# Optimization experiments

Hardware: AMD Instinct MI355X
Metric: run time of the kernel (lower is better)

## Reference

```python
import jax, jax.numpy as jnp
import numpy as np

N, E = 100000, 1600000
IN_DIM, HID, NCLS = 64, 128, 18
BATCH, K = 8, 5000


def setup_inputs() -> dict:
    key = jax.random.key(0)
    ks = jax.random.split(key, 9)
    features = jax.random.normal(ks[0], (N, IN_DIM), dtype=jnp.float32)
    src = jax.random.randint(ks[1], (E,), 0, N, dtype=jnp.int32)
    dst = jax.random.randint(ks[2], (E,), 0, N, dtype=jnp.int32)
    def glorot(k, shape):
        lim = float(np.sqrt(6.0 / (shape[0] + shape[1])))
        return jax.random.uniform(k, shape, jnp.float32, -lim, lim)
    W1 = glorot(ks[3], (IN_DIM, HID)); b1 = jnp.zeros((HID,), jnp.float32)
    W2 = glorot(ks[4], (HID, HID));    b2 = jnp.zeros((HID,), jnp.float32)
    W3 = glorot(ks[5], (K * HID, NCLS)); b3 = jnp.zeros((NCLS,), jnp.float32)
    return {"features": features, "src": src, "dst": dst,
            "W1": W1, "b1": b1, "W2": W2, "b2": b2, "W3": W3, "b3": b3}


def reference(features, src, dst, W1, b1, W2, b2, W3, b3):
    n = features.shape[0]
    ones = jnp.ones(src.shape[0], features.dtype)
    out_deg = jax.ops.segment_sum(ones, src, num_segments=n)
    in_deg = jax.ops.segment_sum(ones, dst, num_segments=n)
    norm_src = jnp.clip(out_deg, 1.0) ** -0.5  # DGL norm='both'
    norm_dst = jnp.clip(in_deg, 1.0) ** -0.5

    def gconv(x, W, b, act):
        h = (x @ W) * norm_src[:, None]          # transform then normalize src
        agg = jax.ops.segment_sum(h[src], dst, num_segments=n)  # gather+scatter-add
        agg = agg * norm_dst[:, None] + b
        return jax.nn.relu(agg) if act else agg

    h = gconv(features, W1, b1, True)   # [N, HID]
    h = gconv(h, W2, b2, True)          # [N, HID]

    # global_sort_pool: equal-sized graphs of N//BATCH nodes, top-K by last channel
    n_per = n // BATCH
    hb = h.reshape(BATCH, n_per, HID)
    _, idx = jax.lax.top_k(hb[..., -1], K)                  # [B, K] descending
    topk = jnp.take_along_axis(hb, idx[..., None], axis=1)  # [B, K, HID]
    pooled = topk.reshape(BATCH, K * HID)

    return pooled @ W3 + b3  # [B, NCLS]
```

## Files before the change

### kernel.cpp

```cpp
#include <hip/hip_runtime.h>
#include <cstdint>
#include <cstddef>

#define N_NODES 100000
#define N_EDGES 1600000
#define IN_DIM  64
#define HID     128
#define NCLS    18
#define BATCH   8
#define TOPK    5000
#define NPER    12500
#define SORTN   16384
#define SORTC   2048

#define BSHIFT  9
#define BNODES  (1 << BSHIFT)
#define NBUCK   ((N_NODES + BNODES - 1) / BNODES)
#define CHUNK   8192


__global__ __launch_bounds__(256) void k_bcount(const int* __restrict__ src,
                                                const int* __restrict__ dst,
                                                int* __restrict__ bcntS,
                                                int* __restrict__ bcntD) {
    __shared__ int cs[NBUCK], cd[NBUCK];
    for (int b = threadIdx.x; b < NBUCK; b += 256) { cs[b] = 0; cd[b] = 0; }
    __syncthreads();
    const int base = blockIdx.x * CHUNK;
    const int end  = min(base + CHUNK, N_EDGES);
    for (int e = base + threadIdx.x; e < end; e += 256) {
        atomicAdd(&cs[src[e] >> BSHIFT], 1);
        atomicAdd(&cd[dst[e] >> BSHIFT], 1);
    }
    __syncthreads();
    for (int b = threadIdx.x; b < NBUCK; b += 256) {
        if (cs[b]) atomicAdd(&bcntS[b], cs[b]);
        if (cd[b]) atomicAdd(&bcntD[b], cd[b]);
    }
}

__global__ void k_bscan(const int* __restrict__ bcntS, const int* __restrict__ bcntD,
                        int* __restrict__ baseS, int* __restrict__ baseD,
                        int* __restrict__ curS, int* __restrict__ curD) {
    if (threadIdx.x == 0 && blockIdx.x == 0) {
        int rs = 0, rd = 0;
        for (int b = 0; b < NBUCK; ++b) {
            baseS[b] = rs; curS[b] = rs; rs += bcntS[b];
            baseD[b] = rd; curD[b] = rd; rd += bcntD[b];
        }
        baseS[NBUCK] = rs; baseD[NBUCK] = rd;
    }
}


__global__ __launch_bounds__(256) void k_bin2(const int* __restrict__ src,
                                              const int* __restrict__ dst,
                                              int* __restrict__ cursorD,
                                              int* __restrict__ cursorS,
                                              unsigned* __restrict__ binbuf,
                                              unsigned* __restrict__ sbin) {
    __shared__ int cD[NBUCK], gD[NBUCK], aD[NBUCK];
    __shared__ int cS[NBUCK], gS[NBUCK], aS[NBUCK];
    const int base = blockIdx.x * CHUNK;
    const int end  = min(base + CHUNK, N_EDGES);
    for (int b = threadIdx.x; b < NBUCK; b += 256) {
        cD[b] = 0; aD[b] = 0; cS[b] = 0; aS[b] = 0;
    }
    __syncthreads();
    for (int e = base + threadIdx.x; e < end; e += 256) {
        atomicAdd(&cD[dst[e] >> BSHIFT], 1);
        atomicAdd(&cS[src[e] >> BSHIFT], 1);
    }
    __syncthreads();
    for (int b = threadIdx.x; b < NBUCK; b += 256) {
        if (cD[b] > 0) gD[b] = atomicAdd(&cursorD[b], cD[b]);
        if (cS[b] > 0) gS[b] = atomicAdd(&cursorS[b], cS[b]);
    }
    __syncthreads();
    for (int e = base + threadIdx.x; e < end; e += 256) {
        int d = dst[e], s = src[e];
        int bd = d >> BSHIFT;
        int od = atomicAdd(&aD[bd], 1);
        binbuf[gD[bd] + od] = ((unsigned)(d & (BNODES - 1)) << 17) | (unsigned)s;
        int bs = s >> BSHIFT;
        int os = atomicAdd(&aS[bs], 1);
        sbin[gS[bs] + os] = (unsigned)(s & (BNODES - 1));
    }
}


__global__ __launch_bounds__(256) void k_hist_all(const unsigned* __restrict__ sbin,
                                                  const int* __restrict__ baseS,
                                                  const unsigned* __restrict__ binbuf,
                                                  const int* __restrict__ baseD,
                                                  float* __restrict__ normS,
                                                  float* __restrict__ normD,
                                                  int* __restrict__ row_ptr,
                                                  int* __restrict__ ssrc) {
    __shared__ int cnt[BNODES];
    __shared__ int tmp[BNODES];
    const int nodeBase = blockIdx.x << BSHIFT;
    for (int t = threadIdx.x; t < BNODES; t += 256) cnt[t] = 0;
    __syncthreads();
    {
        const int beg = baseS[blockIdx.x], end = baseS[blockIdx.x + 1];
        for (int e = beg + threadIdx.x; e < end; e += 256)
            atomicAdd(&cnt[sbin[e]], 1);
    }
    __syncthreads();
    for (int t = threadIdx.x; t < BNODES; t += 256) {
        int node = nodeBase + t;
        if (node < N_NODES)
            normS[node] = 1.0f / sqrtf((float)max(cnt[t], 1));
        cnt[t] = 0;
    }
    __syncthreads();
    const int beg = baseD[blockIdx.x], end = baseD[blockIdx.x + 1];
    for (int e = beg + threadIdx.x; e < end; e += 256)
        atomicAdd(&cnt[binbuf[e] >> 17], 1);
    __syncthreads();
    for (int t = threadIdx.x; t < BNODES; t += 256) {
        int node = nodeBase + t;
        if (node < N_NODES)
            normD[node] = 1.0f / sqrtf((float)max(cnt[t], 1));
    }
    for (int s = 1; s < BNODES; s <<= 1) {
        for (int t = threadIdx.x; t < BNODES; t += 256)
            tmp[t] = (t >= s) ? cnt[t - s] + cnt[t] : cnt[t];
        __syncthreads();
        for (int t = threadIdx.x; t < BNODES; t += 256) cnt[t] = tmp[t];
        __syncthreads();
    }
    for (int t = threadIdx.x; t < BNODES; t += 256) {
        int b = beg + ((t == 0) ? 0 : cnt[t - 1]);
        tmp[t] = b;
        int node = nodeBase + t;
        if (node < N_NODES) row_ptr[node] = b;
    }
    if (blockIdx.x == 0 && threadIdx.x == 0) row_ptr[N_NODES] = N_EDGES;
    __syncthreads();
    for (int e = beg + threadIdx.x; e < end; e += 256) {
        unsigned v = binbuf[e];
        int pos = atomicAdd(&tmp[v >> 17], 1);
        ssrc[pos] = (int)(v & 0x1FFFFu);
    }
}


#define BMT 64
#define BKT 32

template<int KDIM, bool SCALE, bool POST, bool KEYS>
__global__ __launch_bounds__(256) void k_fused(const float* __restrict__ X,
                                               const int* __restrict__ row_ptr,
                                               const int* __restrict__ ssrc,
                                               const float* __restrict__ normSrc,
                                               const float* __restrict__ W,
                                               const float* __restrict__ normD,
                                               const float* __restrict__ bias,
                                               const float* __restrict__ normS_post,
                                               float* __restrict__ keys,
                                               float* __restrict__ out) {
    __shared__ float xs[BMT][KDIM + 4];
    __shared__ float ws[BKT * HID];

    const int tid = threadIdx.x;
    const int rt = blockIdx.x * BMT;

    {
        constexpr int LPN = KDIM / 4;
        constexpr int NCH = 256 / LPN;
        const int w = tid / LPN;
        const int lane = tid % LPN;
        const float4* __restrict__ hv = (const float4*)X;
        #pragma unroll
        for (int c = 0; c < BMT / NCH; ++c) {
            const int row = c * NCH + w;
            const int node = rt + row;
            float4 a4 = make_float4(0.f, 0.f, 0.f, 0.f);
            if (node < N_NODES) {
                const int beg = row_ptr[node], end = row_ptr[node + 1];
                int e = beg;
                for (; e + 4 <= end; e += 4) {
                    int s0 = ssrc[e + 0], s1 = ssrc[e + 1], s2 = ssrc[e + 2], s3 = ssrc[e + 3];
                    float4 v0 = hv[(size_t)s0 * LPN + lane];
                    float4 v1 = hv[(size_t)s1 * LPN + lane];
                    float4 v2 = hv[(size_t)s2 * LPN + lane];
                    float4 v3 = hv[(size_t)s3 * LPN + lane];
                    if constexpr (SCALE) {
                        float n0 = normSrc[s0], n1 = normSrc[s1], n2 = normSrc[s2], n3 = normSrc[s3];
                        a4.x += v0.x * n0; a4.y += v0.y * n0; a4.z += v0.z * n0; a4.w += v0.w * n0;
                        a4.x += v1.x * n1; a4.y += v1.y * n1; a4.z += v1.z * n1; a4.w += v1.w * n1;
                        a4.x += v2.x * n2; a4.y += v2.y * n2; a4.z += v2.z * n2; a4.w += v2.w * n2;
                        a4.x += v3.x * n3; a4.y += v3.y * n3; a4.z += v3.z * n3; a4.w += v3.w * n3;
                    } else {
                        a4.x += v0.x; a4.y += v0.y; a4.z += v0.z; a4.w += v0.w;
                        a4.x += v1.x; a4.y += v1.y; a4.z += v1.z; a4.w += v1.w;
                        a4.x += v2.x; a4.y += v2.y; a4.z += v2.z; a4.w += v2.w;
                        a4.x += v3.x; a4.y += v3.y; a4.z += v3.z; a4.w += v3.w;
                    }
                }
                for (; e < end; ++e) {
                    int s0 = ssrc[e];
                    float4 v0 = hv[(size_t)s0 * LPN + lane];
                    if constexpr (SCALE) {
                        float n0 = normSrc[s0];
                        a4.x += v0.x * n0; a4.y += v0.y * n0; a4.z += v0.z * n0; a4.w += v0.w * n0;
                    } else {
                        a4.x += v0.x; a4.y += v0.y; a4.z += v0.z; a4.w += v0.w;
                    }
                }
            }
            *(float4*)&xs[row][lane * 4] = a4;
        }
    }

    const int tx = tid & 31;
    const int ty = tid >> 5;
    const int col0 = tx * 4;
    const int row0 = ty * 8;

    float acc[8][4];
    #pragma unroll
    for (int r = 0; r < 8; ++r)
        #pragma unroll
        for (int c = 0; c < 4; ++c) acc[r][c] = 0.f;

    for (int k0 = 0; k0 < KDIM; k0 += BKT) {
        __syncthreads();
        {
            const float4* wsrc = (const float4*)(W + (size_t)k0 * HID);
            #pragma unroll
            for (int i = tid; i < BKT * HID / 4; i += 256)
                ((float4*)ws)[i] = wsrc[i];
        }
        __syncthreads();
        #pragma unroll 4
        for (int k = 0; k < BKT; ++k) {
            float4 b = *(const float4*)&ws[k * HID + col0];
            float a[8];
            #pragma unroll
            for (int r = 0; r < 8; ++r) a[r] = xs[row0 + r][k0 + k];
            #pragma unroll
            for (int r = 0; r < 8; ++r) {
                acc[r][0] += a[r] * b.x;
                acc[r][1] += a[r] * b.y;
                acc[r][2] += a[r] * b.z;
                acc[r][3] += a[r] * b.w;
            }
        }
    }

    const float4 bb = *(const float4*)(bias + col0);
    #pragma unroll
    for (int r = 0; r < 8; ++r) {
        int gr = rt + row0 + r;
        if (gr < N_NODES) {
            float nd = normD[gr];
            float4 o;
            o.x = fmaxf(acc[r][0] * nd + bb.x, 0.f);
            o.y = fmaxf(acc[r][1] * nd + bb.y, 0.f);
            o.z = fmaxf(acc[r][2] * nd + bb.z, 0.f);
            o.w = fmaxf(acc[r][3] * nd + bb.w, 0.f);
            if (KEYS && col0 == 124) keys[gr] = o.w;
            if (POST) {
                float ns = normS_post[gr];
                o.x *= ns; o.y *= ns; o.z *= ns; o.w *= ns;
            }
            *(float4*)(out + (size_t)gr * HID + col0) = o;
        }
    }
}


__global__ __launch_bounds__(256) void k_sort_init(const float* __restrict__ keys,
                                                   unsigned long long* __restrict__ arr) {
    int i = blockIdx.x * 256 + threadIdx.x;
    if (i >= BATCH * SORTN) return;
    int g = i >> 14;
    int l = i & (SORTN - 1);
    unsigned long long c;
    if (l < NPER) {
        unsigned u = __float_as_uint(keys[g * NPER + l]);
        unsigned s = (u & 0x80000000u) ? ~u : (u | 0x80000000u);
        unsigned d = ~s;
        c = ((unsigned long long)d << 32) | (unsigned)l;
    } else {
        c = 0xFFFFFFFFFFFFFFFFull;
    }
    arr[i] = c;
}

__global__ __launch_bounds__(1024) void k_sort_local_full(unsigned long long* __restrict__ arr) {
    __shared__ unsigned long long lds[SORTC];
    const int base  = blockIdx.x * SORTC;
    const int gbase = base & (SORTN - 1);
    lds[threadIdx.x]        = arr[base + threadIdx.x];
    lds[threadIdx.x + 1024] = arr[base + threadIdx.x + 1024];
    __syncthreads();
    for (int k = 2; k <= SORTC; k <<= 1) {
        for (int j = k >> 1; j > 0; j >>= 1) {
            int t = threadIdx.x;
            int i = ((t & ~(j - 1)) << 1) | (t & (j - 1));
            bool up = (((gbase + i) & k) == 0);
            unsigned long long a = lds[i], b = lds[i + j];
            if ((a > b) == up) { lds[i] = b; lds[i + j] = a; }
            __syncthreads();
        }
    }
    arr[base + threadIdx.x]        = lds[threadIdx.x];
    arr[base + threadIdx.x + 1024] = lds[threadIdx.x + 1024];
}

__global__ __launch_bounds__(256) void k_sort_global(unsigned long long* __restrict__ arr,
                                                     int k, int j) {
    int tg = blockIdx.x * 256 + threadIdx.x;
    if (tg >= BATCH * (SORTN / 2)) return;
    int g = tg >> 13;
    int t = tg & (SORTN / 2 - 1);
    int i = ((t & ~(j - 1)) << 1) | (t & (j - 1));
    bool up = ((i & k) == 0);
    unsigned long long* p = arr + (size_t)g * SORTN;
    unsigned long long a = p[i], b = p[i + j];
    if ((a > b) == up) { p[i] = b; p[i + j] = a; }
}

__global__ __launch_bounds__(1024) void k_sort_local_tail(unsigned long long* __restrict__ arr,
                                                          int k) {
    __shared__ unsigned long long lds[SORTC];
    const int base  = blockIdx.x * SORTC;
    const int gbase = base & (SORTN - 1);
    lds[threadIdx.x]        = arr[base + threadIdx.x];
    lds[threadIdx.x + 1024] = arr[base + threadIdx.x + 1024];
    __syncthreads();
    for (int j = SORTC >> 1; j > 0; j >>= 1) {
        int t = threadIdx.x;
        int i = ((t & ~(j - 1)) << 1) | (t & (j - 1));
        bool up = (((gbase + i) & k) == 0);
        unsigned long long a = lds[i], b = lds[i + j];
        if ((a > b) == up) { lds[i] = b; lds[i + j] = a; }
        __syncthreads();
    }
    arr[base + threadIdx.x]        = lds[threadIdx.x];
    arr[base + threadIdx.x + 1024] = lds[threadIdx.x + 1024];
}

__global__ __launch_bounds__(256) void k_sort_emit(const unsigned long long* __restrict__ arr,
                                                   int* __restrict__ topk_idx,
                                                   const float* __restrict__ b3,
                                                   float* __restrict__ out) {
    int i = blockIdx.x * 256 + threadIdx.x;
    if (i < BATCH * NCLS) out[i] = b3[i % NCLS];
    if (i >= BATCH * TOPK) return;
    int b = i / TOPK;
    int k = i - b * TOPK;
    topk_idx[i] = (int)(arr[(size_t)b * SORTN + k] & 0xFFFFFFFFull);
}


#define KPB 100

__global__ __launch_bounds__(128) void k_final(const float* __restrict__ h2,
                                               const int* __restrict__ topk_idx,
                                               const float* __restrict__ W3,
                                               float* __restrict__ out) {
    __shared__ float red[128 * NCLS];
    const int b = blockIdx.x / (TOPK / KPB);
    const int chunk = blockIdx.x % (TOPK / KPB);
    const int j = threadIdx.x;
    float acc[NCLS];
    #pragma unroll
    for (int c = 0; c < NCLS; ++c) acc[c] = 0.f;
    const int k0 = chunk * KPB;
    for (int k = k0; k < k0 + KPB; ++k) {
        int node = b * NPER + topk_idx[b * TOPK + k];
        float h = h2[(size_t)node * HID + j];
        const float* wrow = W3 + (size_t)(k * HID + j) * NCLS;
        #pragma unroll
        for (int c = 0; c < NCLS; ++c) acc[c] += h * wrow[c];
    }
    #pragma unroll
    for (int c = 0; c < NCLS; ++c) red[j * NCLS + c] = acc[c];
    __syncthreads();
    for (int s = 64; s > 0; s >>= 1) {
        if (j < s) {
            #pragma unroll
            for (int c = 0; c < NCLS; ++c) red[j * NCLS + c] += red[(j + s) * NCLS + c];
        }
        __syncthreads();
    }
    if (j < NCLS) atomicAdd(&out[b * NCLS + j], red[j]);
}


extern "C" void kernel_launch(void* const* d_in, const int* in_sizes, int n_in,
                              void* d_out, int out_size, void* d_ws, size_t ws_size,
                              hipStream_t stream) {
    const float* features = (const float*)d_in[0];
    const int*   src      = (const int*)d_in[1];
    const int*   dst      = (const int*)d_in[2];
    const float* W1       = (const float*)d_in[3];
    const float* b1       = (const float*)d_in[4];
    const float* W2       = (const float*)d_in[5];
    const float* b2       = (const float*)d_in[6];
    const float* W3       = (const float*)d_in[7];
    const float* b3       = (const float*)d_in[8];
    float* out = (float*)d_out;

    char* p = (char*)d_ws;
    auto carve = [&](size_t bytes) -> void* {
        void* r = (void*)p;
        p += (bytes + 511) & ~(size_t)511;
        return r;
    };
    float* normS     = (float*)carve((size_t)N_NODES * 4);
    float* normD     = (float*)carve((size_t)N_NODES * 4);
    int*   row_ptr   = (int*)carve((size_t)(N_NODES + 1) * 4);
    int*   bcntS     = (int*)carve((size_t)NBUCK * 4);
    int*   bcntD     = (int*)carve((size_t)NBUCK * 4);
    int*   baseS     = (int*)carve((size_t)(NBUCK + 1) * 4);
    int*   baseD     = (int*)carve((size_t)(NBUCK + 1) * 4);
    int*   curS      = (int*)carve((size_t)NBUCK * 4);
    int*   curD      = (int*)carve((size_t)NBUCK * 4);
    int*   ssrc      = (int*)carve((size_t)N_EDGES * 4);
    unsigned* binbuf = (unsigned*)carve((size_t)N_EDGES * 4);
    unsigned* sbin   = (unsigned*)carve((size_t)N_EDGES * 4);
    float* keys      = (float*)carve((size_t)N_NODES * 4);
    int*   topk_idx  = (int*)carve((size_t)BATCH * TOPK * 4);
    unsigned long long* sortbuf = (unsigned long long*)carve((size_t)BATCH * SORTN * 8);
    float* bufA      = (float*)carve((size_t)N_NODES * HID * 4);
    float* bufB      = (float*)carve((size_t)N_NODES * HID * 4);

    const int GB = (N_NODES + BMT - 1) / BMT;
    const int BB = (N_EDGES + CHUNK - 1) / CHUNK;

    hipMemsetAsync(bcntS, 0, (size_t)NBUCK * 4, stream);
    hipMemsetAsync(bcntD, 0, (size_t)NBUCK * 4, stream);

    k_bcount<<<BB, 256, 0, stream>>>(src, dst, bcntS, bcntD);
    k_bscan<<<1, 64, 0, stream>>>(bcntS, bcntD, baseS, baseD, curS, curD);
    k_bin2<<<BB, 256, 0, stream>>>(src, dst, curD, curS, binbuf, sbin);
    k_hist_all<<<NBUCK, 256, 0, stream>>>(sbin, baseS, binbuf, baseD,
                                          normS, normD, row_ptr, ssrc);

    k_fused<IN_DIM, true, true, false><<<GB, 256, 0, stream>>>(
        features, row_ptr, ssrc, normS, W1, normD, b1, normS, nullptr, bufA);
    k_fused<HID, false, false, true><<<GB, 256, 0, stream>>>(
        bufA, row_ptr, ssrc, nullptr, W2, normD, b2, nullptr, keys, bufB);

    const int NCHUNK = BATCH * SORTN / SORTC;
    const int GCE    = (BATCH * (SORTN / 2) + 255) / 256;
    k_sort_init<<<(BATCH * SORTN + 255) / 256, 256, 0, stream>>>(keys, sortbuf);
    k_sort_local_full<<<NCHUNK, 1024, 0, stream>>>(sortbuf);
    k_sort_global<<<GCE, 256, 0, stream>>>(sortbuf, 4096, 2048);
    k_sort_local_tail<<<NCHUNK, 1024, 0, stream>>>(sortbuf, 4096);
    k_sort_global<<<GCE, 256, 0, stream>>>(sortbuf, 8192, 4096);
    k_sort_global<<<GCE, 256, 0, stream>>>(sortbuf, 8192, 2048);
    k_sort_local_tail<<<NCHUNK, 1024, 0, stream>>>(sortbuf, 8192);
    k_sort_global<<<GCE, 256, 0, stream>>>(sortbuf, 16384, 8192);
    k_sort_global<<<GCE, 256, 0, stream>>>(sortbuf, 16384, 4096);
    k_sort_global<<<GCE, 256, 0, stream>>>(sortbuf, 16384, 2048);
    k_sort_local_tail<<<NCHUNK, 1024, 0, stream>>>(sortbuf, 16384);
    k_sort_emit<<<(BATCH * TOPK + 255) / 256, 256, 0, stream>>>(sortbuf, topk_idx, b3, out);

    k_final<<<BATCH * (TOPK / KPB), 128, 0, stream>>>(bufB, topk_idx, W3, out);
}
```

Before: 583.6 us.

## Split layer-2 fused aggregate+GEMM into separate gather kernel and tiled GEMM

The second graph conv layer previously ran as one fused kernel in which each 64-node block gathered neighbor rows into shared memory and then multiplied by W2. It is now split into a warp-per-node aggregation kernel writing to a global buffer, followed by a standalone tiled GEMM that applies the norm, bias and ReLU and extracts the sort keys. This gives the irregular gather its own launch shape, with small blocks and more parallelism, and avoids the large shared-memory tile that limited occupancy in the fused version. The cost is an extra round trip of the 100000x128 aggregated tensor through global memory, plus one more launch.

Measured after the change: 578.4 us. About the same (-0.9%).

```diff
diff --git a/kernel.cpp b/kernel.cpp
--- a/kernel.cpp
+++ b/kernel.cpp
@@ -150,25 +150,22 @@
 #define BMT 64
 #define BKT 32
 
-template<int KDIM, bool SCALE, bool POST, bool KEYS>
-__global__ __launch_bounds__(256) void k_fused(const float* __restrict__ X,
-                                               const int* __restrict__ row_ptr,
-                                               const int* __restrict__ ssrc,
-                                               const float* __restrict__ normSrc,
-                                               const float* __restrict__ W,
-                                               const float* __restrict__ normD,
-                                               const float* __restrict__ bias,
-                                               const float* __restrict__ normS_post,
-                                               float* __restrict__ keys,
-                                               float* __restrict__ out) {
-    __shared__ float xs[BMT][KDIM + 4];
+__global__ __launch_bounds__(256) void k_fused1(const float* __restrict__ X,
+                                                const int* __restrict__ row_ptr,
+                                                const int* __restrict__ ssrc,
+                                                const float* __restrict__ normS,
+                                                const float* __restrict__ W,
+                                                const float* __restrict__ normD,
+                                                const float* __restrict__ bias,
+                                                float* __restrict__ out) {
+    __shared__ float xs[BMT][IN_DIM + 4];
     __shared__ float ws[BKT * HID];
 
     const int tid = threadIdx.x;
     const int rt = blockIdx.x * BMT;
 
     {
-        constexpr int LPN = KDIM / 4;
+        constexpr int LPN = IN_DIM / 4;
         constexpr int NCH = 256 / LPN;
         const int w = tid / LPN;
         const int lane = tid % LPN;
@@ -183,32 +180,21 @@
                 int e = beg;
                 for (; e + 4 <= end; e += 4) {
                     int s0 = ssrc[e + 0], s1 = ssrc[e + 1], s2 = ssrc[e + 2], s3 = ssrc[e + 3];
+                    float n0 = normS[s0], n1 = normS[s1], n2 = normS[s2], n3 = normS[s3];
                     float4 v0 = hv[(size_t)s0 * LPN + lane];
                     float4 v1 = hv[(size_t)s1 * LPN + lane];
                     float4 v2 = hv[(size_t)s2 * LPN + lane];
                     float4 v3 = hv[(size_t)s3 * LPN + lane];
-                    if constexpr (SCALE) {
-                        float n0 = normSrc[s0], n1 = normSrc[s1], n2 = normSrc[s2], n3 = normSrc[s3];
-                        a4.x += v0.x * n0; a4.y += v0.y * n0; a4.z += v0.z * n0; a4.w += v0.w * n0;
-                        a4.x += v1.x * n1; a4.y += v1.y * n1; a4.z += v1.z * n1; a4.w += v1.w * n1;
-                        a4.x += v2.x * n2; a4.y += v2.y * n2; a4.z += v2.z * n2; a4.w += v2.w * n2;
-                        a4.x += v3.x * n3; a4.y += v3.y * n3; a4.z += v3.z * n3; a4.w += v3.w * n3;
-                    } else {
-                        a4.x += v0.x; a4.y += v0.y; a4.z += v0.z; a4.w += v0.w;
-                        a4.x += v1.x; a4.y += v1.y; a4.z += v1.z; a4.w += v1.w;
-                        a4.x += v2.x; a4.y += v2.y; a4.z += v2.z; a4.w += v2.w;
-                        a4.x += v3.x; a4.y += v3.y; a4.z += v3.z; a4.w += v3.w;
-                    }
+                    a4.x += v0.x * n0; a4.y += v0.y * n0; a4.z += v0.z * n0; a4.w += v0.w * n0;
+                    a4.x += v1.x * n1; a4.y += v1.y * n1; a4.z += v1.z * n1; a4.w += v1.w * n1;
+                    a4.x += v2.x * n2; a4.y += v2.y * n2; a4.z += v2.z * n2; a4.w += v2.w * n2;
+                    a4.x += v3.x * n3; a4.y += v3.y * n3; a4.z += v3.z * n3; a4.w += v3.w * n3;
                 }
                 for (; e < end; ++e) {
                     int s0 = ssrc[e];
+                    float n0 = normS[s0];
                     float4 v0 = hv[(size_t)s0 * LPN + lane];
-                    if constexpr (SCALE) {
-                        float n0 = normSrc[s0];
-                        a4.x += v0.x * n0; a4.y += v0.y * n0; a4.z += v0.z * n0; a4.w += v0.w * n0;
-                    } else {
-                        a4.x += v0.x; a4.y += v0.y; a4.z += v0.z; a4.w += v0.w;
-                    }
+                    a4.x += v0.x * n0; a4.y += v0.y * n0; a4.z += v0.z * n0; a4.w += v0.w * n0;
                 }
             }
             *(float4*)&xs[row][lane * 4] = a4;
@@ -226,7 +212,7 @@
         #pragma unroll
         for (int c = 0; c < 4; ++c) acc[r][c] = 0.f;
 
-    for (int k0 = 0; k0 < KDIM; k0 += BKT) {
+    for (int k0 = 0; k0 < IN_DIM; k0 += BKT) {
         __syncthreads();
         {
             const float4* wsrc = (const float4*)(W + (size_t)k0 * HID);
@@ -262,11 +248,115 @@
             o.y = fmaxf(acc[r][1] * nd + bb.y, 0.f);
             o.z = fmaxf(acc[r][2] * nd + bb.z, 0.f);
             o.w = fmaxf(acc[r][3] * nd + bb.w, 0.f);
-            if (KEYS && col0 == 124) keys[gr] = o.w;
-            if (POST) {
-                float ns = normS_post[gr];
-                o.x *= ns; o.y *= ns; o.z *= ns; o.w *= ns;
+            float ns = normS[gr];
+            o.x *= ns; o.y *= ns; o.z *= ns; o.w *= ns;
+            *(float4*)(out + (size_t)gr * HID + col0) = o;
+        }
+    }
+}
+
+
+#define ACC4(A, V) { A.x += V.x; A.y += V.y; A.z += V.z; A.w += V.w; }
+
+__global__ __launch_bounds__(256) void k_agg128(const float* __restrict__ hs,
+                                                const int* __restrict__ row_ptr,
+                                                const int* __restrict__ ssrc,
+                                                float* __restrict__ out) {
+    const int node = blockIdx.x * 8 + (threadIdx.x >> 5);
+    const int lane = threadIdx.x & 31;
+    if (node >= N_NODES) return;
+    const int beg = row_ptr[node], end = row_ptr[node + 1];
+    const float4* __restrict__ hv = (const float4*)hs;
+    float4 acc = make_float4(0.f, 0.f, 0.f, 0.f);
+    int e = beg;
+    for (; e + 4 <= end; e += 4) {
+        int s0 = ssrc[e + 0], s1 = ssrc[e + 1], s2 = ssrc[e + 2], s3 = ssrc[e + 3];
+        float4 v0 = hv[(size_t)s0 * 32 + lane];
+        float4 v1 = hv[(size_t)s1 * 32 + lane];
+        float4 v2 = hv[(size_t)s2 * 32 + lane];
+        float4 v3 = hv[(size_t)s3 * 32 + lane];
+        ACC4(acc, v0); ACC4(acc, v1); ACC4(acc, v2); ACC4(acc, v3);
+    }
+    for (; e < end; ++e) {
+        float4 v0 = hv[(size_t)ssrc[e] * 32 + lane];
+        ACC4(acc, v0);
+    }
+    *(float4*)(out + (size_t)node * HID + lane * 4) = acc;
+}
+
+
+__global__ __launch_bounds__(256) void k_gemm2(const float* __restrict__ X,
+                                               const float* __restrict__ W,
+                                               const float* __restrict__ normD,
+                                               const float* __restrict__ bias,
+                                               float* __restrict__ keys,
+                                               float* __restrict__ out) {
+    __shared__ float xs[BMT][BKT + 4];
+    __shared__ float ws[BKT * HID];
+
+    const int tid = threadIdx.x;
+    const int tx = tid & 31;
+    const int ty = tid >> 5;
+    const int col0 = tx * 4;
+    const int row0 = ty * 8;
+    const int rt = blockIdx.x * BMT;
+
+    float acc[8][4];
+    #pragma unroll
+    for (int r = 0; r < 8; ++r)
+        #pragma unroll
+        for (int c = 0; c < 4; ++c) acc[r][c] = 0.f;
+
+    for (int k0 = 0; k0 < HID; k0 += BKT) {
+        __syncthreads();
+        {
+            const float4* wsrc = (const float4*)(W + (size_t)k0 * HID);
+            #pragma unroll
+            for (int i = tid; i < BKT * HID / 4; i += 256)
+                ((float4*)ws)[i] = wsrc[i];
+        }
+        {
+            #pragma unroll
+            for (int i = tid; i < BMT * BKT / 4; i += 256) {
+                int row = i >> 3;
+                int kq  = i & 7;
+                int gr  = rt + row;
+                float4 v = make_float4(0.f, 0.f, 0.f, 0.f);
+                if (gr < N_NODES)
+                    v = *(const float4*)(X + (size_t)gr * HID + k0 + kq * 4);
+                *(float4*)&xs[row][kq * 4] = v;
             }
+        }
+        __syncthreads();
+
+        #pragma unroll 4
+        for (int k = 0; k < BKT; ++k) {
+            float4 b = *(const float4*)&ws[k * HID + col0];
+            float a[8];
+            #pragma unroll
+            for (int r = 0; r < 8; ++r) a[r] = xs[row0 + r][k];
+            #pragma unroll
+            for (int r = 0; r < 8; ++r) {
+                acc[r][0] += a[r] * b.x;
+                acc[r][1] += a[r] * b.y;
+                acc[r][2] += a[r] * b.z;
+                acc[r][3] += a[r] * b.w;
+            }
+        }
+    }
+
+    const float4 bb = *(const float4*)(bias + col0);
+    #pragma unroll
+    for (int r = 0; r < 8; ++r) {
+        int gr = rt + row0 + r;
+        if (gr < N_NODES) {
+            float nd = normD[gr];
+            float4 o;
+            o.x = fmaxf(acc[r][0] * nd + bb.x, 0.f);
+            o.y = fmaxf(acc[r][1] * nd + bb.y, 0.f);
+            o.z = fmaxf(acc[r][2] * nd + bb.z, 0.f);
+            o.w = fmaxf(acc[r][3] * nd + bb.w, 0.f);
+            if (col0 == 124) keys[gr] = o.w;
             *(float4*)(out + (size_t)gr * HID + col0) = o;
         }
     }
@@ -443,10 +533,9 @@
     k_hist_all<<<NBUCK, 256, 0, stream>>>(sbin, baseS, binbuf, baseD,
                                           normS, normD, row_ptr, ssrc);
 
-    k_fused<IN_DIM, true, true, false><<<GB, 256, 0, stream>>>(
-        features, row_ptr, ssrc, normS, W1, normD, b1, normS, nullptr, bufA);
-    k_fused<HID, false, false, true><<<GB, 256, 0, stream>>>(
-        bufA, row_ptr, ssrc, nullptr, W2, normD, b2, nullptr, keys, bufB);
+    k_fused1<<<GB, 256, 0, stream>>>(features, row_ptr, ssrc, normS, W1, normD, b1, bufA);
+    k_agg128<<<(N_NODES + 7) / 8, 256, 0, stream>>>(bufA, row_ptr, ssrc, bufB);
+    k_gemm2<<<GB, 256, 0, stream>>>(bufB, W2, normD, b2, keys, bufA);
 
     const int NCHUNK = BATCH * SORTN / SORTC;
     const int GCE    = (BATCH * (SORTN / 2) + 255) / 256;
@@ -463,5 +552,5 @@
     k_sort_local_tail<<<NCHUNK, 1024, 0, stream>>>(sortbuf, 16384);
     k_sort_emit<<<(BATCH * TOPK + 255) / 256, 256, 0, stream>>>(sortbuf, topk_idx, b3, out);
 
-    k_final<<<BATCH * (TOPK / KPB), 128, 0, stream>>>(bufB, topk_idx, W3, out);
-}
+    k_final<<<BATCH * (TOPK / KPB), 128, 0, stream>>>(bufA, topk_idx, W3, out);
+}
```
